# Performance work log

Hardware: AMD Instinct MI355X
Metric: run time of the kernel (lower is better)

## Reference

```python
import jax, jax.numpy as jnp
import numpy as np

SIGMA = 0.05
KSIZE = 3
MIN_VAL = 50.0
MAX_VAL = 100.0


def _gauss_kernel():
    # ax = range(-(3//2)+1, 3//2+1) = [-1, 0, 1]  (matches TF int-floor-div)
    ax = jnp.arange(-(KSIZE // 2) + 1.0, KSIZE // 2 + 1.0)
    xx, yy = jnp.meshgrid(ax, ax)
    k = jnp.exp(-(xx ** 2 + yy ** 2) / (2.0 * SIGMA ** 2))
    k = k / jnp.sum(k)
    return k[..., None, None].astype(jnp.float32)  # HWIO, C=1


def _reflect_pad(x):
    return jnp.pad(x, ((0, 0), (1, 1), (1, 1), (0, 0)), mode='reflect')


def _conv(x, k):
    return jax.lax.conv_general_dilated(x, k, (1, 1), 'VALID',
                                        dimension_numbers=('NHWC', 'HWIO', 'NHWC'))


def _canny(images):
    blur = _conv(_reflect_pad(images), _gauss_kernel())
    h = jnp.array([[-1, 0, 1], [-2, 0, 2], [-1, 0, 1]], jnp.float32)[..., None, None]
    v = jnp.array([[-1, -2, -1], [0, 0, 0], [1, 2, 1]], jnp.float32)[..., None, None]
    bp = _reflect_pad(blur)
    gx = _conv(bp, h)
    gy = _conv(bp, v)
    gxy = jnp.sqrt(gx ** 2 + gy ** 2)
    # NOTE: original uses atan2(gx, gy) in this arg order
    theta = (jnp.arctan2(gx, gy) * (180.0 / np.pi) + 90.0) % 180.0

    H, W = gx.shape[1], gx.shape[2]
    # dilation2d with a -inf/0 kernel == max over the kernel's zero-offsets of the
    # zero-padded image; offsets are (dy,dx) of the 0 entries of each 3x3 filter.
    offsets = [
        [(1, 0), (1, 1), (1, 2)],  # horizontal bin: middle row
        [(0, 2), (1, 1), (2, 0)],  # 45 deg: anti-diagonal
        [(0, 1), (1, 1), (2, 1)],  # vertical bin: middle column
        [(0, 0), (1, 1), (2, 2)],  # 135 deg: main diagonal
    ]
    conds = [
        jnp.logical_or(theta >= 157.5, theta < 22.5),
        jnp.logical_and(theta >= 22.5, theta < 67.5),
        jnp.logical_and(theta >= 67.5, theta < 112.5),
        jnp.logical_and(theta >= 112.5, theta < 157.5),
    ]

    edge = jnp.zeros_like(gxy)
    for cond, offs in zip(conds, offsets):
        ang = jnp.where(cond, gxy, 0.0)
        pad = jnp.pad(ang, ((0, 0), (1, 1), (1, 1), (0, 0)))  # zero pad, as ZeroPadding2D
        mp = pad[:, offs[0][0]:offs[0][0] + H, offs[0][1]:offs[0][1] + W, :]
        for dy, dx in offs[1:]:
            mp = jnp.maximum(mp, pad[:, dy:dy + H, dx:dx + W, :])
        edge = edge + jnp.where(mp == ang, ang, 0.0)

    edge_sure = jnp.where(edge >= MAX_VAL, 255.0, 0.0)
    edge_week = jnp.where(jnp.logical_and(edge >= MIN_VAL, edge < MAX_VAL), 255.0, 0.0)
    edge_image = jnp.where(jnp.logical_or(edge_week == 255.0, edge_sure == 255.0), 255.5, 0.0)
    return edge_image, edge_week, edge_sure


def setup_inputs() -> dict:
    key = jax.random.key(0)
    images = jax.random.uniform(key, (16, 1024, 1024, 1), dtype=jnp.float32) * 255.0
    return {"images": images}


def reference(images):
    return _canny(images)
```

## Files before the change

### kernel.cpp

```cpp
#include <hip/hip_runtime.h>
#include <math.h>

#define IMG_H 1024
#define IMG_W 1024
#define OUT_H 1025
#define OUT_W 1025
#define NIMG  16
#define TOTAL ((size_t)NIMG * OUT_H * OUT_W)

#define TILE_W 64
#define TILE_H 16
#define HALO_W 68
#define HALO_H 18
#define NQX    17
#define NQUAD  (HALO_H * NQX)
#define NTHREADS 320

__device__ __forceinline__ int refl(int k) {
    if (k >= 2) return (k <= 1025) ? (k - 2) : 1022;
    return k;
}

__device__ __forceinline__ void sobel_generic(const float* __restrict__ img, int i, int j,
                                              float& gx, float& gy) {
    int r0 = refl(i), r1 = refl(i + 1), r2 = refl(i + 2);
    int c0 = refl(j), c1 = refl(j + 1), c2 = refl(j + 2);
    const float* p0 = img + r0 * IMG_W;
    const float* p1 = img + r1 * IMG_W;
    const float* p2 = img + r2 * IMG_W;
    float v00 = p0[c0], v01 = p0[c1], v02 = p0[c2];
    float v10 = p1[c0],               v12 = p1[c2];
    float v20 = p2[c0], v21 = p2[c1], v22 = p2[c2];

    float t = -v00;
    t = __fadd_rn(t, v02);
    t = __fadd_rn(t, -2.0f * v10);
    t = __fadd_rn(t, 2.0f * v12);
    t = __fadd_rn(t, -v20);
    gx = __fadd_rn(t, v22);

    t = -v00;
    t = __fadd_rn(t, -2.0f * v01);
    t = __fadd_rn(t, -v02);
    t = __fadd_rn(t, v20);
    t = __fadd_rn(t, 2.0f * v21);
    gy = __fadd_rn(t, v22);
}

__device__ int classify_slow(float gx, float gy) {
    float t = (float)atan2((double)gx, (double)gy);
    float deg = __fmul_rn(t, (float)(180.0 / M_PI));
    float th = __fadd_rn(deg, 90.0f);
    th = fmodf(th, 180.0f);
    if (th < 0.0f) th += 180.0f;
    if (th < 22.5f || th >= 157.5f) return 0;
    if (th < 67.5f) return 1;
    if (th < 112.5f) return 2;
    return 3;
}

__device__ __forceinline__ int classify(float gx, float gy) {
    float ax = fabsf(gx), ay = fabsf(gy);
    const float T22_LO = 0.414172141e0f;
    const float T22_HI = 0.414254984e0f;
    const float T67_LO = 2.413972141e0f;
    const float T67_HI = 2.414454984e0f;

    bool in22 = (ax > ay * T22_LO) && (ax < ay * T22_HI);
    bool in67 = (ax > ay * T67_LO) && (ax < ay * T67_HI);
    if (__builtin_expect(in22 || in67, 0))
        return classify_slow(gx, gy);

    unsigned s = (__float_as_uint(gx) ^ __float_as_uint(gy)) >> 31;
    int diag = s ? 1 : 3;
    return (ax <= ay * T22_LO) ? 2 : ((ax >= ay * T67_HI) ? 0 : diag);
}

__device__ __forceinline__ float mag(float gx, float gy) {
    return __fsqrt_rn(__fadd_rn(__fmul_rn(gx, gx), __fmul_rn(gy, gy)));
}

__device__ __forceinline__ void load6(const float* __restrict__ p, float v[6]) {
    float4 a = *(const float4*)p;
    float2 b = *(const float2*)(p + 4);
    v[0] = a.x; v[1] = a.y; v[2] = a.z; v[3] = a.w; v[4] = b.x; v[5] = b.y;
}

__global__ __launch_bounds__(NTHREADS) void canny_kernel(const float* __restrict__ images,
                                                         float* __restrict__ out) {
    __shared__ float    g_s[HALO_H * HALO_W];
    __shared__ unsigned b_u[HALO_H * NQX];

    const int tile_ox = blockIdx.x * TILE_W;
    const int tile_oy = blockIdx.y * TILE_H;
    const int n       = blockIdx.z;
    const float* img = images + (size_t)n * IMG_H * IMG_W;
    const int t = threadIdx.x;

    if (t < NQUAD) {
        int hy  = t / NQX;
        int qx  = t - hy * NQX;
        int oy  = tile_oy + hy - 1;
        int ox0 = tile_ox + qx * 4 - 2;

        float    gq[4];
        unsigned bq[4];

        if (oy >= 2 && oy <= 1023 && ox0 >= 2 && ox0 <= 1020) {
            const float* r0p = img + (oy - 2) * IMG_W + (ox0 - 2);
            float R0[6], R1[6], R2[6];
            load6(r0p, R0);
            load6(r0p + IMG_W, R1);
            load6(r0p + 2 * IMG_W, R2);
            #pragma unroll
            for (int p = 0; p < 4; p++) {
                float v00 = R0[p], v01 = R0[p + 1], v02 = R0[p + 2];
                float v10 = R1[p],                  v12 = R1[p + 2];
                float v20 = R2[p], v21 = R2[p + 1], v22 = R2[p + 2];

                float s = -v00;
                s = __fadd_rn(s, v02);
                s = __fadd_rn(s, -2.0f * v10);
                s = __fadd_rn(s, 2.0f * v12);
                s = __fadd_rn(s, -v20);
                float gx = __fadd_rn(s, v22);

                s = -v00;
                s = __fadd_rn(s, -2.0f * v01);
                s = __fadd_rn(s, -v02);
                s = __fadd_rn(s, v20);
                s = __fadd_rn(s, 2.0f * v21);
                float gy = __fadd_rn(s, v22);

                gq[p] = mag(gx, gy);
                bq[p] = (unsigned)classify(gx, gy);
            }
        } else {
            #pragma unroll
            for (int p = 0; p < 4; p++) {
                int ox = ox0 + p;
                float g = -1.0f;
                unsigned b = 255u;
                if (oy >= 0 && oy < OUT_H && ox >= 0 && ox < OUT_W) {
                    float gx, gy;
                    sobel_generic(img, oy, ox, gx, gy);
                    g = mag(gx, gy);
                    b = (unsigned)classify(gx, gy);
                }
                gq[p] = g;
                bq[p] = b;
            }
        }

        int ldoff = hy * HALO_W + qx * 4;
        *(float4*)&g_s[ldoff] = make_float4(gq[0], gq[1], gq[2], gq[3]);
        b_u[hy * NQX + qx] = bq[0] | (bq[1] << 8) | (bq[2] << 16) | (bq[3] << 24);
    }
    __syncthreads();

    const unsigned char* b_s = (const unsigned char*)b_u;
    float* const out_i = out;
    float* const out_w = out + TOTAL;
    float* const out_s = out + 2 * TOTAL;
    #pragma unroll
    for (int q = 0; q < 4; q++) {
        int p = t + NTHREADS * q;
        if (p >= TILE_W * TILE_H) break;
        int r = p >> 6, c = p & 63;
        int oy = tile_oy + r, ox = tile_ox + c;
        if (oy >= OUT_H || ox >= OUT_W) continue;

        int hc = (r + 1) * HALO_W + (c + 2);
        float gc = g_s[hc];
        int   bc = b_s[hc];

        int doff = (bc == 0) ? 1
                 : (bc == 1) ? (HALO_W - 1)
                 : (bc == 2) ? HALO_W
                 :             (HALO_W + 1);

        float nmax = 0.0f;
        float g1 = g_s[hc + doff];
        if (b_s[hc + doff] == bc && g1 > nmax) nmax = g1;
        float g2 = g_s[hc - doff];
        if (b_s[hc - doff] == bc && g2 > nmax) nmax = g2;

        float e = (gc >= nmax) ? gc : 0.0f;

        size_t o = (size_t)(n * OUT_H + oy) * OUT_W + ox;
        __builtin_nontemporal_store((e >= 50.0f) ? 255.5f : 0.0f, out_i + o);
        __builtin_nontemporal_store((e >= 50.0f && e < 100.0f) ? 255.0f : 0.0f, out_w + o);
        __builtin_nontemporal_store((e >= 100.0f) ? 255.0f : 0.0f, out_s + o);
    }
}

extern "C" void kernel_launch(void* const* d_in, const int* in_sizes, int n_in,
                              void* d_out, int out_size, void* d_ws, size_t ws_size,
                              hipStream_t stream) {
    const float* images = (const float*)d_in[0];
    float* out = (float*)d_out;
    dim3 grid((OUT_W + TILE_W - 1) / TILE_W,
              (OUT_H + TILE_H - 1) / TILE_H,
              NIMG);
    canny_kernel<<<grid, NTHREADS, 0, stream>>>(images, out);
}
```

Before: 298.4 us.

## Process four row-tiles per block with double-buffered LDS and register prefetch

Each block now walks four vertically stacked 64x16 tiles, keeping two LDS buffers and prefetching the next tile's input rows into registers while the current tile's non-max suppression and stores run. The goal is to overlap global loads with compute and output stores, and to cut the number of blocks launched. The output stores also change from nontemporal to ordinary stores, which may alter cache behaviour on the write-heavy path. The cost is fewer blocks, so less parallelism, and more registers per thread.

```diff
diff --git a/kernel.cpp b/kernel.cpp
--- a/kernel.cpp
+++ b/kernel.cpp
@@ -10,6 +10,7 @@
 
 #define TILE_W 64
 #define TILE_H 16
+#define NTILES 4
 #define HALO_W 68
 #define HALO_H 18
 #define NQX    17
@@ -88,109 +89,138 @@
 
 __global__ __launch_bounds__(NTHREADS) void canny_kernel(const float* __restrict__ images,
                                                          float* __restrict__ out) {
-    __shared__ float    g_s[HALO_H * HALO_W];
-    __shared__ unsigned b_u[HALO_H * NQX];
+    __shared__ float    g_s[2][HALO_H * HALO_W];
+    __shared__ unsigned b_u[2][HALO_H * NQX];
 
     const int tile_ox = blockIdx.x * TILE_W;
-    const int tile_oy = blockIdx.y * TILE_H;
+    const int base_oy = blockIdx.y * (TILE_H * NTILES);
     const int n       = blockIdx.z;
     const float* img = images + (size_t)n * IMG_H * IMG_W;
     const int t = threadIdx.x;
 
-    if (t < NQUAD) {
-        int hy  = t / NQX;
-        int qx  = t - hy * NQX;
-        int oy  = tile_oy + hy - 1;
-        int ox0 = tile_ox + qx * 4 - 2;
-
-        float    gq[4];
-        unsigned bq[4];
-
-        if (oy >= 2 && oy <= 1023 && ox0 >= 2 && ox0 <= 1020) {
-            const float* r0p = img + (oy - 2) * IMG_W + (ox0 - 2);
-            float R0[6], R1[6], R2[6];
-            load6(r0p, R0);
-            load6(r0p + IMG_W, R1);
-            load6(r0p + 2 * IMG_W, R2);
-            #pragma unroll
-            for (int p = 0; p < 4; p++) {
-                float v00 = R0[p], v01 = R0[p + 1], v02 = R0[p + 2];
-                float v10 = R1[p],                  v12 = R1[p + 2];
-                float v20 = R2[p], v21 = R2[p + 1], v22 = R2[p + 2];
-
-                float s = -v00;
-                s = __fadd_rn(s, v02);
-                s = __fadd_rn(s, -2.0f * v10);
-                s = __fadd_rn(s, 2.0f * v12);
-                s = __fadd_rn(s, -v20);
-                float gx = __fadd_rn(s, v22);
-
-                s = -v00;
-                s = __fadd_rn(s, -2.0f * v01);
-                s = __fadd_rn(s, -v02);
-                s = __fadd_rn(s, v20);
-                s = __fadd_rn(s, 2.0f * v21);
-                float gy = __fadd_rn(s, v22);
-
-                gq[p] = mag(gx, gy);
-                bq[p] = (unsigned)classify(gx, gy);
-            }
-        } else {
-            #pragma unroll
-            for (int p = 0; p < 4; p++) {
-                int ox = ox0 + p;
-                float g = -1.0f;
-                unsigned b = 255u;
-                if (oy >= 0 && oy < OUT_H && ox >= 0 && ox < OUT_W) {
-                    float gx, gy;
-                    sobel_generic(img, oy, ox, gx, gy);
-                    g = mag(gx, gy);
-                    b = (unsigned)classify(gx, gy);
-                }
-                gq[p] = g;
-                bq[p] = b;
-            }
-        }
-
-        int ldoff = hy * HALO_W + qx * 4;
-        *(float4*)&g_s[ldoff] = make_float4(gq[0], gq[1], gq[2], gq[3]);
-        b_u[hy * NQX + qx] = bq[0] | (bq[1] << 8) | (bq[2] << 16) | (bq[3] << 24);
-    }
-    __syncthreads();
-
-    const unsigned char* b_s = (const unsigned char*)b_u;
+    const int hy  = t / NQX;
+    const int qx  = t - hy * NQX;
+    const int ox0 = tile_ox + qx * 4 - 2;
+
     float* const out_i = out;
     float* const out_w = out + TOTAL;
     float* const out_s = out + 2 * TOTAL;
-    #pragma unroll
-    for (int q = 0; q < 4; q++) {
-        int p = t + NTHREADS * q;
-        if (p >= TILE_W * TILE_H) break;
-        int r = p >> 6, c = p & 63;
-        int oy = tile_oy + r, ox = tile_ox + c;
-        if (oy >= OUT_H || ox >= OUT_W) continue;
-
-        int hc = (r + 1) * HALO_W + (c + 2);
-        float gc = g_s[hc];
-        int   bc = b_s[hc];
-
-        int doff = (bc == 0) ? 1
-                 : (bc == 1) ? (HALO_W - 1)
-                 : (bc == 2) ? HALO_W
-                 :             (HALO_W + 1);
-
-        float nmax = 0.0f;
-        float g1 = g_s[hc + doff];
-        if (b_s[hc + doff] == bc && g1 > nmax) nmax = g1;
-        float g2 = g_s[hc - doff];
-        if (b_s[hc - doff] == bc && g2 > nmax) nmax = g2;
-
-        float e = (gc >= nmax) ? gc : 0.0f;
-
-        size_t o = (size_t)(n * OUT_H + oy) * OUT_W + ox;
-        __builtin_nontemporal_store((e >= 50.0f) ? 255.5f : 0.0f, out_i + o);
-        __builtin_nontemporal_store((e >= 50.0f && e < 100.0f) ? 255.0f : 0.0f, out_w + o);
-        __builtin_nontemporal_store((e >= 100.0f) ? 255.0f : 0.0f, out_s + o);
+
+    float F0[6], F1[6], F2[6];
+    bool  pf_int = false;
+
+    if (t < NQUAD) {
+        int oy = base_oy + hy - 1;
+        pf_int = (oy >= 2 && oy <= 1023 && ox0 >= 2 && ox0 <= 1020);
+        if (pf_int) {
+            const float* rp = img + (oy - 2) * IMG_W + (ox0 - 2);
+            load6(rp, F0);
+            load6(rp + IMG_W, F1);
+            load6(rp + 2 * IMG_W, F2);
+        }
+    }
+
+    int cur = 0;
+    for (int tt = 0; tt < NTILES; ++tt) {
+        const int tile_oy = base_oy + tt * TILE_H;
+        const bool live = (tile_oy < OUT_H);
+
+        if (live && t < NQUAD) {
+            int oy = tile_oy + hy - 1;
+            float    gq[4];
+            unsigned bq[4];
+            if (pf_int) {
+                #pragma unroll
+                for (int p = 0; p < 4; p++) {
+                    float v00 = F0[p], v01 = F0[p + 1], v02 = F0[p + 2];
+                    float v10 = F1[p],                  v12 = F1[p + 2];
+                    float v20 = F2[p], v21 = F2[p + 1], v22 = F2[p + 2];
+
+                    float s = -v00;
+                    s = __fadd_rn(s, v02);
+                    s = __fadd_rn(s, -2.0f * v10);
+                    s = __fadd_rn(s, 2.0f * v12);
+                    s = __fadd_rn(s, -v20);
+                    float gx = __fadd_rn(s, v22);
+
+                    s = -v00;
+                    s = __fadd_rn(s, -2.0f * v01);
+                    s = __fadd_rn(s, -v02);
+                    s = __fadd_rn(s, v20);
+                    s = __fadd_rn(s, 2.0f * v21);
+                    float gy = __fadd_rn(s, v22);
+
+                    gq[p] = mag(gx, gy);
+                    bq[p] = (unsigned)classify(gx, gy);
+                }
+            } else {
+                #pragma unroll
+                for (int p = 0; p < 4; p++) {
+                    int ox = ox0 + p;
+                    float g = -1.0f;
+                    unsigned b = 255u;
+                    if (oy >= 0 && oy < OUT_H && ox >= 0 && ox < OUT_W) {
+                        float gx, gy;
+                        sobel_generic(img, oy, ox, gx, gy);
+                        g = mag(gx, gy);
+                        b = (unsigned)classify(gx, gy);
+                    }
+                    gq[p] = g;
+                    bq[p] = b;
+                }
+            }
+            int ldoff = hy * HALO_W + qx * 4;
+            *(float4*)&g_s[cur][ldoff] = make_float4(gq[0], gq[1], gq[2], gq[3]);
+            b_u[cur][hy * NQX + qx] = bq[0] | (bq[1] << 8) | (bq[2] << 16) | (bq[3] << 24);
+        }
+        __syncthreads();
+
+        if (tt + 1 < NTILES && (tile_oy + TILE_H) < OUT_H && t < NQUAD) {
+            int oy = tile_oy + TILE_H + hy - 1;
+            pf_int = (oy >= 2 && oy <= 1023 && ox0 >= 2 && ox0 <= 1020);
+            if (pf_int) {
+                const float* rp = img + (oy - 2) * IMG_W + (ox0 - 2);
+                load6(rp, F0);
+                load6(rp + IMG_W, F1);
+                load6(rp + 2 * IMG_W, F2);
+            }
+        }
+
+        if (live) {
+            const float* gs = g_s[cur];
+            const unsigned char* b_s = (const unsigned char*)b_u[cur];
+            #pragma unroll
+            for (int q = 0; q < 4; q++) {
+                int p = t + NTHREADS * q;
+                if (p >= TILE_W * TILE_H) break;
+                int r = p >> 6, c = p & 63;
+                int oy = tile_oy + r, ox = tile_ox + c;
+                if (oy >= OUT_H || ox >= OUT_W) continue;
+
+                int hc = (r + 1) * HALO_W + (c + 2);
+                float gc = gs[hc];
+                int   bc = b_s[hc];
+
+                int doff = (bc == 0) ? 1
+                         : (bc == 1) ? (HALO_W - 1)
+                         : (bc == 2) ? HALO_W
+                         :             (HALO_W + 1);
+
+                float nmax = 0.0f;
+                float g1 = gs[hc + doff];
+                if (b_s[hc + doff] == bc && g1 > nmax) nmax = g1;
+                float g2 = gs[hc - doff];
+                if (b_s[hc - doff] == bc && g2 > nmax) nmax = g2;
+
+                float e = (gc >= nmax) ? gc : 0.0f;
+
+                size_t o = (size_t)(n * OUT_H + oy) * OUT_W + ox;
+                out_i[o] = (e >= 50.0f) ? 255.5f : 0.0f;
+                out_w[o] = (e >= 50.0f && e < 100.0f) ? 255.0f : 0.0f;
+                out_s[o] = (e >= 100.0f) ? 255.0f : 0.0f;
+            }
+        }
+        cur ^= 1;
     }
 }
 
@@ -200,7 +230,7 @@
     const float* images = (const float*)d_in[0];
     float* out = (float*)d_out;
     dim3 grid((OUT_W + TILE_W - 1) / TILE_W,
-              (OUT_H + TILE_H - 1) / TILE_H,
+              (OUT_H + TILE_H * NTILES - 1) / (TILE_H * NTILES),
               NIMG);
     canny_kernel<<<grid, NTHREADS, 0, stream>>>(images, out);
 }
```

After: 433.8 us. 45.4% more time.

## Shrink tiles to 64x10 with 128 threads, interleave magnitude and bin in LDS

Applied to the files above, without the earlier changes.

Reduces the tile height from 16 to 10 rows and the block size from 320 to 128 threads, and asks for 8 blocks per SIMD through launch bounds. The halo compute now runs as a strided loop over quads. Magnitude and direction bin are packed into one float2 LDS array, so each neighbor needs one load, and the neighbor max uses fmaxf instead of branches. Output stores switch from nontemporal to normal stores. The smaller tiles raise the share of recomputed halo rows, from 2 of 16 to 2 of 10.

```diff
diff --git a/kernel.cpp b/kernel.cpp
--- a/kernel.cpp
+++ b/kernel.cpp
@@ -9,12 +9,12 @@
 #define TOTAL ((size_t)NIMG * OUT_H * OUT_W)
 
 #define TILE_W 64
-#define TILE_H 16
+#define TILE_H 10
 #define HALO_W 68
-#define HALO_H 18
+#define HALO_H 12
 #define NQX    17
 #define NQUAD  (HALO_H * NQX)
-#define NTHREADS 320
+#define NTHREADS 128
 
 __device__ __forceinline__ int refl(int k) {
     if (k >= 2) return (k <= 1025) ? (k - 2) : 1022;
@@ -86,10 +86,9 @@
     v[0] = a.x; v[1] = a.y; v[2] = a.z; v[3] = a.w; v[4] = b.x; v[5] = b.y;
 }
 
-__global__ __launch_bounds__(NTHREADS) void canny_kernel(const float* __restrict__ images,
-                                                         float* __restrict__ out) {
-    __shared__ float    g_s[HALO_H * HALO_W];
-    __shared__ unsigned b_u[HALO_H * NQX];
+__global__ __launch_bounds__(NTHREADS, 8) void canny_kernel(const float* __restrict__ images,
+                                                            float* __restrict__ out) {
+    __shared__ float2 gb_s[HALO_H * HALO_W];
 
     const int tile_ox = blockIdx.x * TILE_W;
     const int tile_oy = blockIdx.y * TILE_H;
@@ -97,9 +96,9 @@
     const float* img = images + (size_t)n * IMG_H * IMG_W;
     const int t = threadIdx.x;
 
-    if (t < NQUAD) {
-        int hy  = t / NQX;
-        int qx  = t - hy * NQX;
+    for (int idx = t; idx < NQUAD; idx += NTHREADS) {
+        int hy  = idx / NQX;
+        int qx  = idx - hy * NQX;
         int oy  = tile_oy + hy - 1;
         int ox0 = tile_ox + qx * 4 - 2;
 
@@ -152,45 +151,45 @@
             }
         }
 
-        int ldoff = hy * HALO_W + qx * 4;
-        *(float4*)&g_s[ldoff] = make_float4(gq[0], gq[1], gq[2], gq[3]);
-        b_u[hy * NQX + qx] = bq[0] | (bq[1] << 8) | (bq[2] << 16) | (bq[3] << 24);
+        float2* dst = &gb_s[hy * HALO_W + qx * 4];
+        dst[0] = make_float2(gq[0], __uint_as_float(bq[0]));
+        dst[1] = make_float2(gq[1], __uint_as_float(bq[1]));
+        dst[2] = make_float2(gq[2], __uint_as_float(bq[2]));
+        dst[3] = make_float2(gq[3], __uint_as_float(bq[3]));
     }
     __syncthreads();
 
-    const unsigned char* b_s = (const unsigned char*)b_u;
     float* const out_i = out;
     float* const out_w = out + TOTAL;
     float* const out_s = out + 2 * TOTAL;
     #pragma unroll
-    for (int q = 0; q < 4; q++) {
+    for (int q = 0; q < (TILE_W * TILE_H) / NTHREADS; q++) {
         int p = t + NTHREADS * q;
-        if (p >= TILE_W * TILE_H) break;
         int r = p >> 6, c = p & 63;
         int oy = tile_oy + r, ox = tile_ox + c;
         if (oy >= OUT_H || ox >= OUT_W) continue;
 
         int hc = (r + 1) * HALO_W + (c + 2);
-        float gc = g_s[hc];
-        int   bc = b_s[hc];
+        float2 cb = gb_s[hc];
+        float    gc = cb.x;
+        unsigned bc = __float_as_uint(cb.y);
 
         int doff = (bc == 0) ? 1
                  : (bc == 1) ? (HALO_W - 1)
                  : (bc == 2) ? HALO_W
                  :             (HALO_W + 1);
 
-        float nmax = 0.0f;
-        float g1 = g_s[hc + doff];
-        if (b_s[hc + doff] == bc && g1 > nmax) nmax = g1;
-        float g2 = g_s[hc - doff];
-        if (b_s[hc - doff] == bc && g2 > nmax) nmax = g2;
-
+        float2 nb1 = gb_s[hc + doff];
+        float2 nb2 = gb_s[hc - doff];
+        float m1 = (__float_as_uint(nb1.y) == bc) ? nb1.x : 0.0f;
+        float m2 = (__float_as_uint(nb2.y) == bc) ? nb2.x : 0.0f;
+        float nmax = fmaxf(m1, m2);
         float e = (gc >= nmax) ? gc : 0.0f;
 
         size_t o = (size_t)(n * OUT_H + oy) * OUT_W + ox;
-        __builtin_nontemporal_store((e >= 50.0f) ? 255.5f : 0.0f, out_i + o);
-        __builtin_nontemporal_store((e >= 50.0f && e < 100.0f) ? 255.0f : 0.0f, out_w + o);
-        __builtin_nontemporal_store((e >= 100.0f) ? 255.0f : 0.0f, out_s + o);
+        out_i[o] = (e >= 50.0f) ? 255.5f : 0.0f;
+        out_w[o] = (e >= 50.0f && e < 100.0f) ? 255.0f : 0.0f;
+        out_s[o] = (e >= 100.0f) ? 255.0f : 0.0f;
     }
 }
 
```

Measured after the change: 351.0 us. 1.18x slower.
